# Performance work log

Hardware: AMD Instinct MI355X
Metric: run time of the kernel (lower is better)

The kernel has to match this reference:

```python
import jax, jax.numpy as jnp
import numpy as np

NUM_LAYERS = 4
UNITS = 512
DX = 8e-6
WAVELENGTHS = np.array([4.5e-7, 5.32e-7, 6.33e-7], dtype=np.float32)
Z_LAYERS = 0.03
Z_PROP = 0.05
NUM_MODES = 16
BASE_IDX = 1  # base_wavelength_idx in source


def setup_inputs() -> dict:
    key = jax.random.key(0)
    k1, k2 = jax.random.split(key)
    C = len(WAVELENGTHS)
    x = jax.random.normal(k1, (NUM_MODES, C, UNITS, UNITS), dtype=jnp.float32)
    # phase = rand(units, units) * pi, one per layer
    phases = jax.random.uniform(k2, (NUM_LAYERS, UNITS, UNITS), dtype=jnp.float32) * np.pi
    # wavelength_coefficients initialized to base_wavelength / wl (learned params)
    base = WAVELENGTHS[BASE_IDX]
    coeffs = jnp.tile(jnp.asarray(base / WAVELENGTHS, dtype=jnp.float32), (NUM_LAYERS, 1))
    lams = jnp.asarray(WAVELENGTHS)
    return {"x": x, "phases": phases, "coeffs": coeffs, "lams": lams}


def _transfer_fn(lams, z, n, dx):
    # Band-limited angular-spectrum transfer function, per wavelength: [C, H, W]
    f = jnp.fft.fftfreq(n, d=dx).astype(jnp.float32)
    fx2 = f[None, :] ** 2 + f[:, None] ** 2          # [H, W]
    arg = (1.0 / lams)[:, None, None] ** 2 - fx2[None]  # [C, H, W]
    valid = arg > 0
    kz = 2.0 * jnp.pi * jnp.sqrt(jnp.where(valid, arg, 0.0))
    return jnp.where(valid, jnp.exp(1j * (kz * z).astype(jnp.float32)), 0.0)


def _propagate(field, Hf):
    # field: [B, C, H, W] complex; Hf: [C, H, W] — batched angular-spectrum step
    return jnp.fft.ifft2(jnp.fft.fft2(field) * Hf[None])


def reference(x, phases, coeffs, lams):
    n = x.shape[-1]
    H_layer = _transfer_fn(lams, Z_LAYERS, n, DX)  # inter-layer propagation
    H_final = _transfer_fn(lams, Z_PROP, n, DX)    # propagation to detector
    field = x.astype(jnp.complex64)
    for l in range(NUM_LAYERS):
        # per-wavelength effective phase: phase * coeff (depth_factor == 1)
        eff = phases[l][None, :, :] * coeffs[l][:, None, None]  # [C, H, W]
        field = field * jnp.exp(1j * eff)[None]
        field = _propagate(field, H_layer)
    field = _propagate(field, H_final)
    return jnp.abs(field) ** 2
```

## Files before the change

### kernel.cpp

```cpp
#include <hip/hip_runtime.h>
#include <hip/hip_fp16.h>
#include <math.h>


#define TWOPI_F 6.2831854820251465f
#define RSQ2    0.70710678f
#define NPIX    (48*512*512)

__device__ __forceinline__ float2 cadd(float2 a, float2 b){ return make_float2(a.x+b.x, a.y+b.y); }
__device__ __forceinline__ float2 csub(float2 a, float2 b){ return make_float2(a.x-b.x, a.y-b.y); }
__device__ __forceinline__ float2 cmul(float2 a, float2 b){ return make_float2(a.x*b.x - a.y*b.y, a.x*b.y + a.y*b.x); }

template<int S> __device__ __forceinline__ float2 mul_i(float2 a){
  return (S>0) ? make_float2(-a.y, a.x) : make_float2(a.y, -a.x);
}
template<int S> __device__ __forceinline__ float2 mul_w1(float2 a){
  return (S>0) ? make_float2(RSQ2*(a.x-a.y), RSQ2*(a.x+a.y))
               : make_float2(RSQ2*(a.x+a.y), RSQ2*(a.y-a.x));
}
template<int S> __device__ __forceinline__ float2 mul_w3(float2 a){
  return (S>0) ? make_float2(RSQ2*(-a.x-a.y), RSQ2*(a.x-a.y))
               : make_float2(RSQ2*(a.y-a.x), RSQ2*(-a.x-a.y));
}
template<int S> __device__ __forceinline__ float2 cmul_tw(float2 v, float2 w){
  float wy = (S>0) ? -w.y : w.y;
  return make_float2(v.x*w.x - v.y*wy, v.x*wy + v.y*w.x);
}

template<int S>
__device__ __forceinline__ void dft8(const float2* a, float2* d){
  float2 b0=cadd(a[0],a[4]), b1=cadd(a[1],a[5]), b2=cadd(a[2],a[6]), b3=cadd(a[3],a[7]);
  float2 b4=csub(a[0],a[4]);
  float2 b5=mul_w1<S>(csub(a[1],a[5]));
  float2 b6=mul_i<S> (csub(a[2],a[6]));
  float2 b7=mul_w3<S>(csub(a[3],a[7]));
  float2 c0=cadd(b0,b2), c2=csub(b0,b2);
  float2 c1=cadd(b1,b3), c3=mul_i<S>(csub(b1,b3));
  float2 c4=cadd(b4,b6), c6=csub(b4,b6);
  float2 c5=cadd(b5,b7), c7=mul_i<S>(csub(b5,b7));
  d[0]=cadd(c0,c1); d[1]=csub(c0,c1);
  d[2]=cadd(c2,c3); d[3]=csub(c2,c3);
  d[4]=cadd(c4,c5); d[5]=csub(c4,c5);
  d[6]=cadd(c6,c7); d[7]=csub(c6,c7);
}

__device__ __forceinline__ int SWZR(int i){ return i ^ ((i>>4)&7); }

__device__ __forceinline__ void lds_fence(){ asm volatile("s_waitcnt lgkmcnt(0)" ::: "memory"); }

__device__ __forceinline__ void make_tw(int t, float2* tw0, float2* tw1){
  float sn, cs;
  __sincosf((TWOPI_F/512.0f)*(float)t, &sn, &cs);
  float2 w0 = make_float2(cs, -sn);
  tw0[0] = make_float2(1.0f, 0.0f);
  #pragma unroll
  for(int k=1;k<8;k++) tw0[k] = cmul(tw0[k-1], w0);
  int p = t>>3;
  __sincosf((TWOPI_F/64.0f)*(float)p, &sn, &cs);
  float2 w1 = make_float2(cs, -sn);
  tw1[0] = make_float2(1.0f, 0.0f);
  #pragma unroll
  for(int k=1;k<8;k++) tw1[k] = cmul(tw1[k-1], w1);
}

template<int S>
__device__ __forceinline__ void fft512_wv(float2* a, float2* o, float2* B, int t,
                                          float scale, const float2* tw0, const float2* tw1){
  const int km[8] = {0,4,2,6,1,5,3,7};
  float2 d[8];
  dft8<S>(a, d);
  #pragma unroll
  for(int k=0;k<8;k++)
    B[SWZR(8*t+k)] = (k==0) ? d[0] : cmul_tw<S>(d[km[k]], tw0[k]);
  lds_fence();
  #pragma unroll
  for(int r=0;r<8;r++) a[r] = B[SWZR(t+64*r)];
  lds_fence();
  dft8<S>(a, d);
  {
    int p = t>>3, q = t&7;
    #pragma unroll
    for(int k=0;k<8;k++)
      B[SWZR(q + 64*p + 8*k)] = (k==0) ? d[0] : cmul_tw<S>(d[km[k]], tw1[k]);
  }
  lds_fence();
  #pragma unroll
  for(int r=0;r<8;r++) a[r] = B[SWZR(t+64*r)];
  lds_fence();
  dft8<S>(a, d);
  #pragma unroll
  for(int k=0;k<8;k++) o[k] = make_float2(d[km[k]].x*scale, d[km[k]].y*scale);
}

template<int S, int LD>
__device__ __forceinline__ void fft512_1b(float2* a, float2* o, float2* B, int t,
                                          float scale, const float2* tw0, const float2* tw1){
  const int km[8] = {0,4,2,6,1,5,3,7};
  float2 d[8];
  dft8<S>(a, d);
  #pragma unroll
  for(int k=0;k<8;k++)
    B[(8*t+k)*LD] = (k==0) ? d[0] : cmul_tw<S>(d[km[k]], tw0[k]);
  __syncthreads();
  #pragma unroll
  for(int r=0;r<8;r++) a[r] = B[(t+64*r)*LD];
  __syncthreads();
  dft8<S>(a, d);
  {
    int p = t>>3, q = t&7;
    #pragma unroll
    for(int k=0;k<8;k++)
      B[(q + 64*p + 8*k)*LD] = (k==0) ? d[0] : cmul_tw<S>(d[km[k]], tw1[k]);
  }
  __syncthreads();
  #pragma unroll
  for(int r=0;r<8;r++) a[r] = B[(t+64*r)*LD];
  dft8<S>(a, d);
  #pragma unroll
  for(int k=0;k<8;k++) o[k] = make_float2(d[km[k]].x*scale, d[km[k]].y*scale);
}


struct AccH {
  __half2* p;
  __device__ __forceinline__ float2 ld(int i) const { return __half22float2(p[i]); }
  __device__ __forceinline__ void   st(int i, float2 v) const { p[i] = __floats2half2_rn(v.x, v.y); }
};
struct AccS {
  float* re; float* im;
  __device__ __forceinline__ float2 ld(int i) const { return make_float2(re[i], im[i]); }
  __device__ __forceinline__ void   st(int i, float2 v) const { re[i]=v.x; im[i]=v.y; }
};


__device__ __forceinline__ float2 phase_of(float kz, float zf){
  float tt = __fmul_rn(kz, zf);
  double dt = (double)tt;
  double q  = rint(dt * 0.15915494309189535);
  double rr = fma(-q, 6.283185307179586, dt);
  float sn, cs; __sincosf((float)rr, &sn, &cs);
  return make_float2(cs, sn);
}

__global__ __launch_bounds__(256) void k_htab(const float* __restrict__ lams,
                                              float2* __restrict__ H1, float2* __restrict__ H12){
  int e = blockIdx.x*256 + threadIdx.x;
  int c = e >> 18, fy = (e>>9)&511, col = e&511;
  const float lam = lams[c];
  const float il  = 1.0f / lam;
  const float il2 = __fmul_rn(il, il);
  const float DEN = (float)(512.0 * 8e-6);
  int   sx  = (col < 256) ? col : col - 512;
  int   sy  = (fy  < 256) ? fy  : fy  - 512;
  float fxv = (float)sx / DEN, fyv = (float)sy / DEN;
  float arg = __fsub_rn(il2, __fadd_rn(__fmul_rn(fxv,fxv), __fmul_rn(fyv,fyv)));
  float2 h1 = make_float2(0.0f,0.0f), h12 = h1;
  if(arg > 0.0f){
    float s  = (float)sqrt((double)arg);
    float kz = __fmul_rn(6.2831854820251465f, s);
    h1  = phase_of(kz, 0.03f);
    h12 = cmul(h1, phase_of(kz, 0.05f));
  }
  H1[e] = h1; H12[e] = h12;
}


template<class Acc>
__global__ __launch_bounds__(256) void k_row_first(
    const float* __restrict__ x, Acc f,
    const float* __restrict__ phases, const float* __restrict__ coeffs)
{
  __shared__ float2 lds[4][512];
  const int w = threadIdx.x >> 6, t = threadIdx.x & 63;
  const int img = blockIdx.x, c = img % 3;
  const int row = (blockIdx.y<<2) + w;
  const int base = (img*512 + row)*512;
  const float* ph = phases + row*512;
  const float coeff = coeffs[c];
  float2 tw0[8], tw1[8]; make_tw(t, tw0, tw1);
  float2 a[8], o[8];
  #pragma unroll
  for(int r=0;r<8;r++){
    int i = t + (r<<6);
    float xv = x[base+i];
    float th = __fmul_rn(ph[i], coeff);
    float sn, cs; __sincosf(th, &sn, &cs);
    a[r] = make_float2(xv*cs, xv*sn);
  }
  fft512_wv<-1>(a, o, lds[w], t, 1.0f, tw0, tw1);
  #pragma unroll
  for(int k=0;k<8;k++){ int i=t+(k<<6); f.st(base+i, o[k]); }
}

template<class Acc>
__global__ __launch_bounds__(256) void k_row_mid(
    Acc f, const float* __restrict__ phases, const float* __restrict__ coeffs, int layer)
{
  __shared__ float2 lds[4][512];
  const int w = threadIdx.x >> 6, t = threadIdx.x & 63;
  const int img = blockIdx.x, c = img % 3;
  const int row = (blockIdx.y<<2) + w;
  const int base = (img*512 + row)*512;
  const float* ph = phases + (layer*512 + row)*512;
  const float coeff = coeffs[layer*3 + c];
  float2 tw0[8], tw1[8]; make_tw(t, tw0, tw1);
  float2 a[8], o[8], pv[8];
  #pragma unroll
  for(int r=0;r<8;r++){
    int i=t+(r<<6); a[r]=f.ld(base+i);
    float th = __fmul_rn(ph[i], coeff);
    float sn, cs; __sincosf(th, &sn, &cs);
    pv[r] = make_float2(cs, sn);
  }
  fft512_wv<+1>(a, o, lds[w], t, 1.0f/512.0f, tw0, tw1);
  #pragma unroll
  for(int k=0;k<8;k++) a[k] = cmul(o[k], pv[k]);
  fft512_wv<-1>(a, o, lds[w], t, 1.0f, tw0, tw1);
  #pragma unroll
  for(int k=0;k<8;k++){ int i=t+(k<<6); f.st(base+i, o[k]); }
}

template<class Acc>
__global__ __launch_bounds__(256) void k_row_last(
    Acc f, float* __restrict__ out)
{
  __shared__ float2 lds[4][512];
  const int w = threadIdx.x >> 6, t = threadIdx.x & 63;
  const int img = blockIdx.x;
  const int row = (blockIdx.y<<2) + w;
  const int base = (img*512 + row)*512;
  float2 tw0[8], tw1[8]; make_tw(t, tw0, tw1);
  float2 a[8], o[8];
  #pragma unroll
  for(int r=0;r<8;r++){ int i=t+(r<<6); a[r]=f.ld(base+i); }
  fft512_wv<+1>(a, o, lds[w], t, 1.0f/512.0f, tw0, tw1);
  #pragma unroll
  for(int k=0;k<8;k++){ int i=t+(k<<6); out[base+i] = o[k].x*o[k].x + o[k].y*o[k].y; }
}


template<class Acc, bool TAB>
__global__ __launch_bounds__(512, 4) void k_col8(
    Acc f, const float2* __restrict__ Htab, const float* __restrict__ lams, float z1, float z2)
{
  __shared__ float2 lds[512][9];
  const int cx = threadIdx.x & 7, t = threadIdx.x >> 3;
  const int img = blockIdx.x, c = img % 3;
  const int col = (blockIdx.y<<3) + cx;
  const int ibase = (img<<18) + col;
  float2 tw0[8], tw1[8]; make_tw(t, tw0, tw1);
  float2 a[8], o[8], h[8];
  #pragma unroll
  for(int r=0;r<8;r++){ int gi = ibase + ((t+(r<<6))<<9); a[r]=f.ld(gi); }
  if(TAB){
    const float2* Hrow = Htab + (c<<18) + col;
    #pragma unroll
    for(int k=0;k<8;k++) h[k] = Hrow[(t+(k<<6))<<9];
  } else {
    const float lam = lams[c];
    const float il  = 1.0f / lam;
    const float il2 = __fmul_rn(il, il);
    const float DEN = (float)(512.0 * 8e-6);
    int   sx  = (col < 256) ? col : col - 512;
    float fxv = (float)sx / DEN;
    float fx2 = __fmul_rn(fxv, fxv);
    #pragma unroll
    for(int k=0;k<8;k++){
      int fy = t + (k<<6);
      int sy = (fy < 256) ? fy : fy - 512;
      float fyv = (float)sy / DEN;
      float arg = __fsub_rn(il2, __fadd_rn(fx2, __fmul_rn(fyv,fyv)));
      h[k] = make_float2(0.0f, 0.0f);
      if(arg > 0.0f){
        float s  = (float)sqrt((double)arg);
        float kz = __fmul_rn(6.2831854820251465f, s);
        h[k] = phase_of(kz, z1);
        if(z2 != 0.0f) h[k] = cmul(h[k], phase_of(kz, z2));
      }
    }
  }
  fft512_1b<-1,9>(a, o, &lds[0][cx], t, 1.0f, tw0, tw1);
  #pragma unroll
  for(int k=0;k<8;k++) a[k] = cmul(o[k], h[k]);
  __syncthreads();
  fft512_1b<+1,9>(a, o, &lds[0][cx], t, 1.0f/512.0f, tw0, tw1);
  #pragma unroll
  for(int k=0;k<8;k++){ int gi = ibase + ((t+(k<<6))<<9); f.st(gi, o[k]); }
}


extern "C" void kernel_launch(void* const* d_in, const int* in_sizes, int n_in,
                              void* d_out, int out_size, void* d_ws, size_t ws_size,
                              hipStream_t stream)
{
  const float* x      = (const float*)d_in[0];
  const float* phases = (const float*)d_in[1];
  const float* coeffs = (const float*)d_in[2];
  const float* lams   = (const float*)d_in[3];
  float* out = (float*)d_out;

  const size_t fldH = (size_t)NPIX*4;
  const size_t splB = (size_t)NPIX*4;
  const size_t tabB = (size_t)3*512*512*8;

  dim3 gA(48,128), bA(256);
  dim3 gB(48,64),  bB(512);
  dim3 gH(3*512*512/256), bH(256);

  if(ws_size >= fldH + 2*tabB){
    AccH f { (__half2*)d_ws };
    float2* H1  = (float2*)((char*)d_ws + fldH);
    float2* H12 = H1 + 3*512*512;
    k_htab<<<gH, bH, 0, stream>>>(lams, H1, H12);
    k_row_first<AccH><<<gA, bA, 0, stream>>>(x, f, phases, coeffs);
    for(int l=1; l<=3; l++){
      k_col8<AccH,true><<<gB, bB, 0, stream>>>(f, H1, lams, 0.03f, 0.0f);
      k_row_mid<AccH><<<gA, bA, 0, stream>>>(f, phases, coeffs, l);
    }
    k_col8<AccH,true><<<gB, bB, 0, stream>>>(f, H12, lams, 0.03f, 0.0f);
    k_row_last<AccH><<<gA, bA, 0, stream>>>(f, out);
  } else if(ws_size >= splB + 2*tabB){
    AccS f { out, (float*)d_ws };
    float2* H1  = (float2*)((char*)d_ws + splB);
    float2* H12 = H1 + 3*512*512;
    k_htab<<<gH, bH, 0, stream>>>(lams, H1, H12);
    k_row_first<AccS><<<gA, bA, 0, stream>>>(x, f, phases, coeffs);
    for(int l=1; l<=3; l++){
      k_col8<AccS,true><<<gB, bB, 0, stream>>>(f, H1, lams, 0.03f, 0.0f);
      k_row_mid<AccS><<<gA, bA, 0, stream>>>(f, phases, coeffs, l);
    }
    k_col8<AccS,true><<<gB, bB, 0, stream>>>(f, H12, lams, 0.03f, 0.0f);
    k_row_last<AccS><<<gA, bA, 0, stream>>>(f, out);
  } else {
    AccS f { out, (float*)d_ws };
    k_row_first<AccS><<<gA, bA, 0, stream>>>(x, f, phases, coeffs);
    for(int l=1; l<=3; l++){
      k_col8<AccS,false><<<gB, bB, 0, stream>>>(f, nullptr, lams, 0.03f, 0.0f);
      k_row_mid<AccS><<<gA, bA, 0, stream>>>(f, phases, coeffs, l);
    }
    k_col8<AccS,false><<<gB, bB, 0, stream>>>(f, nullptr, lams, 0.03f, 0.05f);
    k_row_last<AccS><<<gA, bA, 0, stream>>>(f, out);
  }
}
```

Before: 294.3 us.

## Process two adjacent columns per thread in column FFT with float4 vectors

Adds a new column-pass kernel in which each thread handles a pair of adjacent columns packed as float4. Loads and stores of the half-precision field become 8-byte accesses, and the transfer-function table reads become 16-byte accesses. The grid is halved and each block covers 16 columns, using a 64KB LDS buffer with an XOR swizzle. This aims to cut memory-transaction count and reuse twiddle computation across two columns, at the cost of more registers and more LDS, which may lower occupancy.

Result: slower. 324.4 us (+10.3%).

```diff
diff --git a/kernel.cpp b/kernel.cpp
--- a/kernel.cpp
+++ b/kernel.cpp
@@ -25,6 +25,29 @@
 template<int S> __device__ __forceinline__ float2 cmul_tw(float2 v, float2 w){
   float wy = (S>0) ? -w.y : w.y;
   return make_float2(v.x*w.x - v.y*wy, v.x*wy + v.y*w.x);
+}
+
+__device__ __forceinline__ float4 f4add(float4 a, float4 b){ return make_float4(a.x+b.x,a.y+b.y,a.z+b.z,a.w+b.w); }
+__device__ __forceinline__ float4 f4sub(float4 a, float4 b){ return make_float4(a.x-b.x,a.y-b.y,a.z-b.z,a.w-b.w); }
+template<int S> __device__ __forceinline__ float4 mul_i4(float4 a){
+  return (S>0) ? make_float4(-a.y,a.x,-a.w,a.z) : make_float4(a.y,-a.x,a.w,-a.z);
+}
+template<int S> __device__ __forceinline__ float4 mul_w14(float4 a){
+  return (S>0) ? make_float4(RSQ2*(a.x-a.y), RSQ2*(a.x+a.y), RSQ2*(a.z-a.w), RSQ2*(a.z+a.w))
+               : make_float4(RSQ2*(a.x+a.y), RSQ2*(a.y-a.x), RSQ2*(a.z+a.w), RSQ2*(a.w-a.z));
+}
+template<int S> __device__ __forceinline__ float4 mul_w34(float4 a){
+  return (S>0) ? make_float4(RSQ2*(-a.x-a.y), RSQ2*(a.x-a.y), RSQ2*(-a.z-a.w), RSQ2*(a.z-a.w))
+               : make_float4(RSQ2*(a.y-a.x), RSQ2*(-a.x-a.y), RSQ2*(a.w-a.z), RSQ2*(-a.z-a.w));
+}
+template<int S> __device__ __forceinline__ float4 cmul_tw4(float4 v, float2 w){
+  float wy = (S>0) ? -w.y : w.y;
+  return make_float4(v.x*w.x - v.y*wy, v.x*wy + v.y*w.x,
+                     v.z*w.x - v.w*wy, v.z*wy + v.w*w.x);
+}
+__device__ __forceinline__ float4 cmulh4(float4 v, float4 h){
+  return make_float4(v.x*h.x - v.y*h.y, v.x*h.y + v.y*h.x,
+                     v.z*h.z - v.w*h.w, v.z*h.w + v.w*h.z);
 }
 
 template<int S>
@@ -43,8 +66,25 @@
   d[4]=cadd(c4,c5); d[5]=csub(c4,c5);
   d[6]=cadd(c6,c7); d[7]=csub(c6,c7);
 }
+template<int S>
+__device__ __forceinline__ void dft8_4(const float4* a, float4* d){
+  float4 b0=f4add(a[0],a[4]), b1=f4add(a[1],a[5]), b2=f4add(a[2],a[6]), b3=f4add(a[3],a[7]);
+  float4 b4=f4sub(a[0],a[4]);
+  float4 b5=mul_w14<S>(f4sub(a[1],a[5]));
+  float4 b6=mul_i4<S> (f4sub(a[2],a[6]));
+  float4 b7=mul_w34<S>(f4sub(a[3],a[7]));
+  float4 c0=f4add(b0,b2), c2=f4sub(b0,b2);
+  float4 c1=f4add(b1,b3), c3=mul_i4<S>(f4sub(b1,b3));
+  float4 c4=f4add(b4,b6), c6=f4sub(b4,b6);
+  float4 c5=f4add(b5,b7), c7=mul_i4<S>(f4sub(b5,b7));
+  d[0]=f4add(c0,c1); d[1]=f4sub(c0,c1);
+  d[2]=f4add(c2,c3); d[3]=f4sub(c2,c3);
+  d[4]=f4add(c4,c5); d[5]=f4sub(c4,c5);
+  d[6]=f4add(c6,c7); d[7]=f4sub(c6,c7);
+}
 
 __device__ __forceinline__ int SWZR(int i){ return i ^ ((i>>4)&7); }
+__device__ __forceinline__ int CSWZ(int e, int cx){ return (e<<3) + (cx ^ ((e>>3)&7)); }
 
 __device__ __forceinline__ void lds_fence(){ asm volatile("s_waitcnt lgkmcnt(0)" ::: "memory"); }
 
@@ -90,6 +130,35 @@
   dft8<S>(a, d);
   #pragma unroll
   for(int k=0;k<8;k++) o[k] = make_float2(d[km[k]].x*scale, d[km[k]].y*scale);
+}
+
+template<int S>
+__device__ __forceinline__ void fft512_pr(float4* a, float4* o, float4* B, int t, int cx,
+                                          float scale, const float2* tw0, const float2* tw1){
+  const int km[8] = {0,4,2,6,1,5,3,7};
+  float4 d[8];
+  dft8_4<S>(a, d);
+  #pragma unroll
+  for(int k=0;k<8;k++)
+    B[CSWZ(8*t+k, cx)] = (k==0) ? d[0] : cmul_tw4<S>(d[km[k]], tw0[k]);
+  __syncthreads();
+  #pragma unroll
+  for(int r=0;r<8;r++) a[r] = B[CSWZ(t+64*r, cx)];
+  __syncthreads();
+  dft8_4<S>(a, d);
+  {
+    int p = t>>3, q = t&7;
+    #pragma unroll
+    for(int k=0;k<8;k++)
+      B[CSWZ(q + 64*p + 8*k, cx)] = (k==0) ? d[0] : cmul_tw4<S>(d[km[k]], tw1[k]);
+  }
+  __syncthreads();
+  #pragma unroll
+  for(int r=0;r<8;r++) a[r] = B[CSWZ(t+64*r, cx)];
+  dft8_4<S>(a, d);
+  #pragma unroll
+  for(int k=0;k<8;k++)
+    o[k] = make_float4(d[km[k]].x*scale, d[km[k]].y*scale, d[km[k]].z*scale, d[km[k]].w*scale);
 }
 
 template<int S, int LD>
@@ -236,6 +305,49 @@
   fft512_wv<+1>(a, o, lds[w], t, 1.0f/512.0f, tw0, tw1);
   #pragma unroll
   for(int k=0;k<8;k++){ int i=t+(k<<6); out[base+i] = o[k].x*o[k].x + o[k].y*o[k].y; }
+}
+
+
+__global__ __launch_bounds__(512, 4) void k_colp(
+    __half2* __restrict__ F, const float2* __restrict__ Htab, float2* __restrict__ Hdummy)
+{
+  __shared__ float4 lds[512*8];
+  const int cx = threadIdx.x & 7, t = threadIdx.x >> 3;
+  const int img = blockIdx.x, c = img % 3;
+  const int col = (blockIdx.y<<4) + (cx<<1);
+  const int ibase = (img<<18) + col;
+  float2 tw0[8], tw1[8]; make_tw(t, tw0, tw1);
+  float4 a[8], o[8], h[8];
+  #pragma unroll
+  for(int r=0;r<8;r++){
+    int gi = ibase + ((t+(r<<6))<<9);
+    uint2 raw = *reinterpret_cast<const uint2*>(F + gi);
+    __half2 v0, v1;
+    *reinterpret_cast<unsigned int*>(&v0) = raw.x;
+    *reinterpret_cast<unsigned int*>(&v1) = raw.y;
+    float2 fA = __half22float2(v0), fB = __half22float2(v1);
+    a[r] = make_float4(fA.x, fA.y, fB.x, fB.y);
+  }
+  #pragma unroll
+  for(int k=0;k<8;k++){
+    int fy = t + (k<<6);
+    h[k] = *reinterpret_cast<const float4*>(Htab + (c<<18) + (fy<<9) + col);
+  }
+  fft512_pr<-1>(a, o, lds, t, cx, 1.0f, tw0, tw1);
+  #pragma unroll
+  for(int k=0;k<8;k++) a[k] = cmulh4(o[k], h[k]);
+  __syncthreads();
+  fft512_pr<+1>(a, o, lds, t, cx, 1.0f/512.0f, tw0, tw1);
+  #pragma unroll
+  for(int k=0;k<8;k++){
+    int gi = ibase + ((t+(k<<6))<<9);
+    __half2 v0 = __floats2half2_rn(o[k].x, o[k].y);
+    __half2 v1 = __floats2half2_rn(o[k].z, o[k].w);
+    uint2 raw;
+    raw.x = *reinterpret_cast<unsigned int*>(&v0);
+    raw.y = *reinterpret_cast<unsigned int*>(&v1);
+    *reinterpret_cast<uint2*>(F + gi) = raw;
+  }
 }
 
 
@@ -304,6 +416,7 @@
   const size_t tabB = (size_t)3*512*512*8;
 
   dim3 gA(48,128), bA(256);
+  dim3 gP(48,32),  bP(512);
   dim3 gB(48,64),  bB(512);
   dim3 gH(3*512*512/256), bH(256);
 
@@ -314,10 +427,10 @@
     k_htab<<<gH, bH, 0, stream>>>(lams, H1, H12);
     k_row_first<AccH><<<gA, bA, 0, stream>>>(x, f, phases, coeffs);
     for(int l=1; l<=3; l++){
-      k_col8<AccH,true><<<gB, bB, 0, stream>>>(f, H1, lams, 0.03f, 0.0f);
+      k_colp<<<gP, bP, 0, stream>>>((__half2*)d_ws, H1, nullptr);
       k_row_mid<AccH><<<gA, bA, 0, stream>>>(f, phases, coeffs, l);
     }
-    k_col8<AccH,true><<<gB, bB, 0, stream>>>(f, H12, lams, 0.03f, 0.0f);
+    k_colp<<<gP, bP, 0, stream>>>((__half2*)d_ws, H12, nullptr);
     k_row_last<AccH><<<gA, bA, 0, stream>>>(f, out);
   } else if(ws_size >= splB + 2*tabB){
     AccS f { out, (float*)d_ws };
```
